# Optimization experiments

Hardware: AMD Instinct MI355X
Metric: run time of the kernel (lower is better)

## Reference

```python
import jax, jax.numpy as jnp
import numpy as np

N = 100_000   # nodes
C = 32        # classes
E = 3_200_000 # edges


def setup_inputs() -> dict:
    key = jax.random.key(0)
    k1, k2, k3, k4, k5 = jax.random.split(key, 5)
    edge_index = jax.random.randint(k1, (2, E), 0, N, dtype=jnp.int32)
    edge_weight = jax.random.uniform(k2, (E,), dtype=jnp.float32) + 0.1  # positive weights
    inputs = jax.random.normal(k3, (N, C), dtype=jnp.float32)
    labels = jax.random.randint(k4, (N,), 0, C)
    y = jax.nn.one_hot(labels, C, dtype=jnp.float32)  # torch.where(y[:, i]) implies one-hot labels
    sample_mask = jax.random.bernoulli(k5, 0.5, (N,))
    return {"edge_index": edge_index, "edge_weight": edge_weight,
            "inputs": inputs, "y": y, "sample_mask": sample_mask}


def _normalize_sparse(edge_index, edge_weight, n):
    # normalize_sparse_tensor: add self-loops (weight 1), then D^{-1/2} A D^{-1/2}
    loop = jnp.arange(n, dtype=edge_index.dtype)
    row = jnp.concatenate([edge_index[0], loop])
    col = jnp.concatenate([edge_index[1], loop])
    w = jnp.concatenate([edge_weight, jnp.ones((n,), edge_weight.dtype)])
    deg = jax.ops.segment_sum(w, row, num_segments=n)
    dinv = jnp.where(deg > 0, jax.lax.rsqrt(deg), 0.0)
    vals = dinv[row] * w * dinv[col]
    return row, col, vals


def reference(edge_index, edge_weight, inputs, y, sample_mask):
    n, c = inputs.shape
    row, col, vals = _normalize_sparse(edge_index, edge_weight, n)

    p = jax.nn.softmax(inputs, axis=1)
    m = sample_mask.astype(p.dtype)[:, None]
    p = p * (1.0 - m) + y * m          # replace predictions by labels on masked nodes
    ym = y * m                          # labels only on masked nodes

    # nodeH = raw_normed_adj @ p   (sparse spmm)  -> (n, c)
    nodeH = jax.ops.segment_sum(vals[:, None] * p[col], row, num_segments=n)

    # per-class mean of nodeH over nodes with label i (one-hot => sum/count)
    cnt = ym.sum(axis=0)                         # (c,)
    H = (ym.T @ nodeH) / cnt[:, None]            # (c, c); NaN rows if class empty

    # NaN fixups (identity when no NaNs present)
    Hn = jnp.isnan(H)
    H = jnp.where(Hn, H.T, H)
    Hn = jnp.isnan(H)
    H0 = jnp.where(Hn, jnp.zeros_like(H), H)
    miss = (1.0 - H0.sum(axis=1, keepdims=True)) / Hn.sum(axis=1, keepdims=True).astype(H.dtype)
    H = jnp.where(Hn, miss, H0)

    # makeDoubleStochasticH: iterate col-norm then row-norm; 'delta' = ||H||_1 (as in source)
    def cond(state):
        _, i, d = state
        return (d >= 1e-12) & (i < 3000)

    def body(state):
        Hc, i, _ = state
        Hc = Hc / Hc.sum(axis=0, keepdims=True)
        Hc = Hc / Hc.sum(axis=1, keepdims=True)
        return Hc, i + 1, jnp.abs(Hc).sum()

    H, _, _ = jax.lax.while_loop(cond, body, (H, jnp.int32(0), jnp.float32(1e30)))
    return H
```

## Files before the change

### kernel.cpp

```cpp
#include <hip/hip_runtime.h>
#include <hip/hip_fp16.h>


#define RS 40960
#define BDEG 80
#define W 200
#define NBKTMAX 512
#define BCAP 4608
#define LCAP 4096
#define NSC 512
#define NPR NBKTMAX
#define NTOT (1 + NPR)
#define NRED 16
#define RPER ((NTOT + NRED - 1) / NRED)
#define PPAD 204
#define BVW 3200

__global__ __launch_bounds__(1024) void
k_deg(const int* __restrict__ ei, const float* __restrict__ ew,
      __half* __restrict__ slab, const unsigned char* __restrict__ mask_bytes,
      int* __restrict__ flag, float* __restrict__ Hg, float* __restrict__ cnt,
      int* __restrict__ gCnt, int E_, int R, int Nn) {
  __shared__ float h[RS];
  if (blockIdx.x == 0) {
    Hg[threadIdx.x] = 0.f;
    if (threadIdx.x < 32) cnt[threadIdx.x] = 0.f;
    if (threadIdx.x < NBKTMAX) gCnt[threadIdx.x] = 0;
    int* hi = (int*)h;
    if (threadIdx.x == 0) hi[0] = 0;
    __syncthreads();
    int acc = mask_bytes[threadIdx.x * 4 + 1] | mask_bytes[threadIdx.x * 4 + 2]
            | mask_bytes[threadIdx.x * 4 + 3];
    if (acc) atomicOr(&hi[0], 1);
    __syncthreads();
    if (threadIdx.x == 0) *flag = (hi[0] != 0) ? 1 : 0;
  }
  int g = blockIdx.x >> 3, xx = blockIdx.x & 7;
  int r = g % R;
  int sl = xx + 8 * (g / R);
  int lo = r * RS;
  int used = min(RS, Nn - lo);
  for (int i = threadIdx.x; i < used; i += 1024) h[i] = 0.f;
  __syncthreads();
  int Q = E_ >> 2;
  int q0 = (int)((long long)Q * sl / BDEG);
  int q1 = (int)((long long)Q * (sl + 1) / BDEG);
  const int4* ei4 = (const int4*)ei;
  const float4* ew4 = (const float4*)ew;
  int q = q0 + threadIdx.x;
  for (; q + 1024 < q1; q += 2048) {
    int4 ia = ei4[q], ib = ei4[q + 1024];
    float4 wa = ew4[q], wb = ew4[q + 1024];
    unsigned o0 = (unsigned)(ia.x - lo), o1 = (unsigned)(ia.y - lo);
    unsigned o2 = (unsigned)(ia.z - lo), o3 = (unsigned)(ia.w - lo);
    unsigned o4 = (unsigned)(ib.x - lo), o5 = (unsigned)(ib.y - lo);
    unsigned o6 = (unsigned)(ib.z - lo), o7 = (unsigned)(ib.w - lo);
    if (o0 < RS) atomicAdd(&h[o0], wa.x);
    if (o1 < RS) atomicAdd(&h[o1], wa.y);
    if (o2 < RS) atomicAdd(&h[o2], wa.z);
    if (o3 < RS) atomicAdd(&h[o3], wa.w);
    if (o4 < RS) atomicAdd(&h[o4], wb.x);
    if (o5 < RS) atomicAdd(&h[o5], wb.y);
    if (o6 < RS) atomicAdd(&h[o6], wb.z);
    if (o7 < RS) atomicAdd(&h[o7], wb.w);
  }
  for (; q < q1; q += 1024) {
    int4 idx = ei4[q];
    float4 w = ew4[q];
    unsigned o0 = (unsigned)(idx.x - lo), o1 = (unsigned)(idx.y - lo);
    unsigned o2 = (unsigned)(idx.z - lo), o3 = (unsigned)(idx.w - lo);
    if (o0 < RS) atomicAdd(&h[o0], w.x);
    if (o1 < RS) atomicAdd(&h[o1], w.y);
    if (o2 < RS) atomicAdd(&h[o2], w.z);
    if (o3 < RS) atomicAdd(&h[o3], w.w);
  }
  if (sl == BDEG - 1) {
    for (int e = (Q << 2) + threadIdx.x; e < E_; e += 1024) {
      unsigned off = (unsigned)(ei[e] - lo);
      if (off < RS) atomicAdd(&h[off], ew[e]);
    }
  }
  __syncthreads();
  __half* dst = slab + ((size_t)r * BDEG + sl) * RS;
  for (int i = threadIdx.x; i < used; i += 1024) dst[i] = __float2half(h[i]);
}

__global__ void k_node(const float* __restrict__ x, const float* __restrict__ y,
                       const void* __restrict__ maskp, const int* __restrict__ flag,
                       const __half* __restrict__ slab, int2* __restrict__ ninfo,
                       __half* __restrict__ p16, float* __restrict__ Hg,
                       float* __restrict__ cnt, unsigned* __restrict__ bitvec, int Nn) {
  __shared__ float scnt[32], sdiag[32];
  if (threadIdx.x < 32) { scnt[threadIdx.x] = 0.f; sdiag[threadIdx.x] = 0.f; }
  __syncthreads();
  int n = blockIdx.x * blockDim.x + threadIdx.x;
  bool inb = (n < Nn);
  bool byteMask = (*flag != 0);
  bool msk = false;
  if (inb)
    msk = byteMask ? (((const unsigned char*)maskp)[n] != 0)
                   : (((const int*)maskp)[n] != 0);
  unsigned long long bm = __ballot(msk);
  if ((threadIdx.x & 63) == 0)
    ((unsigned long long*)bitvec)[n >> 6] = bm;
  if (inb) {
    const __half* sl = slab + ((size_t)(n / RS) * BDEG) * RS + (n % RS);
    float d = 0.f;
    #pragma unroll 5
    for (int bb = 0; bb < BDEG; ++bb) d += __half2float(sl[(size_t)bb * RS]);
    float dinv = rsqrtf(d + 1.0f);
    int a = -1;
    if (msk) {
      const float4* yi = (const float4*)(y + (size_t)n * 32);
      #pragma unroll
      for (int q = 0; q < 8; ++q) {
        float4 v = yi[q];
        if (v.x == 1.f) a = q * 4 + 0;
        if (v.y == 1.f) a = q * 4 + 1;
        if (v.z == 1.f) a = q * 4 + 2;
        if (v.w == 1.f) a = q * 4 + 3;
      }
      atomicAdd(&scnt[a], 1.f);
      atomicAdd(&sdiag[a], dinv * dinv);
    } else {
      const float4* xi = (const float4*)(x + (size_t)n * 32);
      float xs[32];
      #pragma unroll
      for (int q = 0; q < 8; ++q) {
        float4 v = xi[q];
        xs[q*4+0] = v.x; xs[q*4+1] = v.y; xs[q*4+2] = v.z; xs[q*4+3] = v.w;
      }
      float mx = -3.4e38f;
      #pragma unroll
      for (int i = 0; i < 32; ++i) mx = fmaxf(mx, xs[i]);
      float s = 0.f;
      #pragma unroll
      for (int i = 0; i < 32; ++i) { xs[i] = __expf(xs[i] - mx); s += xs[i]; }
      float inv = 1.f / s;
      union { short sh[32]; int4 v[4]; } u;
      #pragma unroll
      for (int i = 0; i < 32; ++i)
        u.sh[i] = __half_as_short(__float2half(xs[i] * inv));
      int4* po = (int4*)(p16 + (size_t)n * 32);
      #pragma unroll
      for (int q = 0; q < 4; ++q) po[q] = u.v[q];
    }
    int2 ni; ni.x = __float_as_int(dinv); ni.y = a;
    ninfo[n] = ni;
  }
  __syncthreads();
  if (threadIdx.x < 32) {
    if (scnt[threadIdx.x] != 0.f) atomicAdd(&cnt[threadIdx.x], scnt[threadIdx.x]);
    if (sdiag[threadIdx.x] != 0.f) atomicAdd(&Hg[threadIdx.x * 33], sdiag[threadIdx.x]);
  }
}

__global__ __launch_bounds__(1024) void
k_bucket(const int* __restrict__ ei, const float* __restrict__ ew,
         const int2* __restrict__ ninfo, const unsigned* __restrict__ bitvec,
         int2* __restrict__ gBucket, int* __restrict__ gCnt, int E_) {
  __shared__ int2 list[LCAP];
  __shared__ int lcnt;
  __shared__ int bcnt[NBKTMAX];
  __shared__ int gbase[NBKTMAX];
  __shared__ int bplace[NBKTMAX];
  __shared__ unsigned sbv[BVW];
  if (threadIdx.x == 0) lcnt = 0;
  if (threadIdx.x < NBKTMAX) { bcnt[threadIdx.x] = 0; bplace[threadIdx.x] = 0; }
  for (int i = threadIdx.x; i < BVW; i += 1024) sbv[i] = bitvec[i];
  __syncthreads();
  int E4 = E_ >> 2;
  int q0 = (int)((long long)E4 * blockIdx.x / NSC);
  int q1 = (int)((long long)E4 * (blockIdx.x + 1) / NSC);
  for (int q = q0 + threadIdx.x; q < q1; q += 1024) {
    int4 rr = ((const int4*)ei)[q];
    int4 cc = ((const int4*)(ei + E_))[q];
    float4 ww = ((const float4*)ew)[q];
    int rs[4] = {rr.x, rr.y, rr.z, rr.w};
    int cs[4] = {cc.x, cc.y, cc.z, cc.w};
    float wv[4] = {ww.x, ww.y, ww.z, ww.w};
    bool act[4];
    #pragma unroll
    for (int k = 0; k < 4; ++k)
      act[k] = (sbv[(unsigned)rs[k] >> 5] >> (rs[k] & 31)) & 1;
    int2 nr[4];
    #pragma unroll
    for (int k = 0; k < 4; ++k)
      if (act[k]) nr[k] = ninfo[rs[k]];
    #pragma unroll
    for (int k = 0; k < 4; ++k) {
      if (act[k]) {
        float val = __int_as_float(nr[k].x) * wv[k];
        int pos = atomicAdd(&lcnt, 1);
        if (pos < LCAP) list[pos] = make_int2((cs[k] << 5) | nr[k].y, __float_as_int(val));
      }
    }
  }
  if (blockIdx.x == NSC - 1) {
    for (int e = (E4 << 2) + threadIdx.x; e < E_; e += 1024) {
      int r = ei[e];
      if (!((sbv[(unsigned)r >> 5] >> (r & 31)) & 1)) continue;
      int2 nr = ninfo[r];
      int c = ei[E_ + e];
      float val = __int_as_float(nr.x) * ew[e];
      int pos = atomicAdd(&lcnt, 1);
      if (pos < LCAP) list[pos] = make_int2((c << 5) | nr.y, __float_as_int(val));
    }
  }
  __syncthreads();
  int nl = min(lcnt, LCAP);
  for (int i = threadIdx.x; i < nl; i += 1024)
    atomicAdd(&bcnt[(list[i].x >> 5) / W], 1);
  __syncthreads();
  if (threadIdx.x < NBKTMAX) {
    int n = bcnt[threadIdx.x];
    gbase[threadIdx.x] = (n > 0) ? atomicAdd(&gCnt[threadIdx.x], n) : 0;
  }
  __syncthreads();
  for (int i = threadIdx.x; i < nl; i += 1024) {
    int2 rec = list[i];
    int bkt = (rec.x >> 5) / W;
    int slot = atomicAdd(&bplace[bkt], 1);
    int dst = gbase[bkt] + slot;
    if (dst < BCAP) gBucket[(size_t)bkt * BCAP + dst] = rec;
  }
}

__global__ __launch_bounds__(1024) void
k_process(const int2* __restrict__ gBucket, const int* __restrict__ gCnt,
          const int2* __restrict__ ninfo, const __half* __restrict__ p16,
          float* __restrict__ procSlab, int Nn) {
  __shared__ float TlocT[32 * W];
  __shared__ __half plocT[32 * PPAD];
  __shared__ float H32[1024];
  __shared__ float ldin[W];
  __shared__ int   llab[W];
  __shared__ short cmap[W];
  __shared__ short cidx[W];
  __shared__ int   nUs;
  int k = blockIdx.x;
  int c0 = k * W;
  int Wb = min(c0 + W, Nn) - c0;
  H32[threadIdx.x] = 0.f;
  if ((int)threadIdx.x < Wb) {
    int2 ni = ninfo[c0 + threadIdx.x];
    ldin[threadIdx.x] = __int_as_float(ni.x);
    llab[threadIdx.x] = ni.y;
  }
  if (threadIdx.x == 0) nUs = 0;
  __syncthreads();
  if (threadIdx.x < 64) {
    int base = 0;
    for (int ch = 0; ch < W; ch += 64) {
      int j = ch + threadIdx.x;
      bool u = (j < Wb) && (llab[j] < 0);
      unsigned long long m = __ballot(u);
      int p = base + __popcll(m & ((1ull << threadIdx.x) - 1ull));
      if (u) { cmap[j] = (short)p; cidx[p] = (short)j; }
      base += (int)__popcll(m);
    }
    if (threadIdx.x == 0) nUs = base;
  }
  for (int i = threadIdx.x; i < 32 * W; i += 1024) TlocT[i] = 0.f;
  __syncthreads();
  int nU = nUs;
  if (Wb > 0) {
    for (int i = threadIdx.x; i < nU * 32; i += 1024) {
      int j = i >> 5, b = i & 31;
      plocT[b * PPAD + j] = p16[(size_t)(c0 + cidx[j]) * 32 + b];
    }
    int n = min(gCnt[k], BCAP);
    const int2* bk = gBucket + (size_t)k * BCAP;
    for (int i = threadIdx.x; i < n; i += 1024) {
      int2 rec = bk[i];
      int cl = (rec.x >> 5) - c0;
      int a = rec.x & 31;
      float v = __int_as_float(rec.y) * ldin[cl];
      int b = llab[cl];
      if (b >= 0) atomicAdd(&H32[a * 32 + b], v);
      else        atomicAdd(&TlocT[a * W + cmap[cl]], v);
    }
  }
  __syncthreads();
  int a = threadIdx.x >> 5;
  int b = threadIdx.x & 31;
  float acc0 = 0.f, acc1 = 0.f, acc2 = 0.f, acc3 = 0.f;
  int c = 0;
  for (; c + 3 < nU; c += 4) {
    float4 tv = *(const float4*)&TlocT[a * W + c];
    short4 ps = *(const short4*)&plocT[b * PPAD + c];
    acc0 += tv.x * __half2float(__short_as_half(ps.x));
    acc1 += tv.y * __half2float(__short_as_half(ps.y));
    acc2 += tv.z * __half2float(__short_as_half(ps.z));
    acc3 += tv.w * __half2float(__short_as_half(ps.w));
  }
  for (; c < nU; ++c)
    acc0 += TlocT[a * W + c] * __half2float(plocT[b * PPAD + c]);
  procSlab[(size_t)k * 1024 + threadIdx.x] =
      (acc0 + acc1) + (acc2 + acc3) + H32[threadIdx.x];
}

__global__ __launch_bounds__(1024) void
k_red(const float* __restrict__ allSlabs, float* __restrict__ red) {
  int k0 = blockIdx.x * RPER;
  int k1 = min(k0 + RPER, NTOT);
  float s = 0.f;
  for (int k = k0; k < k1; ++k) s += allSlabs[(size_t)k * 1024 + threadIdx.x];
  red[(size_t)blockIdx.x * 1024 + threadIdx.x] = s;
}

__global__ __launch_bounds__(1024) void
k_sinkhorn(const float* __restrict__ red, const float* __restrict__ cnt,
           float* __restrict__ out) {
  __shared__ float sHH[1024];
  int t = threadIdx.x;
  float s = 0.f;
  #pragma unroll
  for (int k = 0; k < NRED; ++k) s += red[(size_t)k * 1024 + t];
  sHH[t] = s;
  __syncthreads();
  int j = t;
  if (j >= 32) return;
  float cj = cnt[j];
  float Hcol[32], Hrow[32];
  #pragma unroll
  for (int i = 0; i < 32; ++i) Hcol[i] = sHH[i * 32 + j];
  #pragma unroll
  for (int i = 0; i < 32; ++i) Hcol[i] /= __shfl(cj, i);
  #pragma unroll
  for (int k = 0; k < 32; ++k) Hrow[k] = sHH[j * 32 + k] / cj;
  float u = 1.f, v = 1.f;
  for (int it = 0; it < 40; ++it) {
    float a0 = 0.f, a1 = 0.f, a2 = 0.f, a3 = 0.f;
    #pragma unroll
    for (int i = 0; i < 32; i += 4) {
      a0 += Hcol[i+0] * __shfl(u, i+0);
      a1 += Hcol[i+1] * __shfl(u, i+1);
      a2 += Hcol[i+2] * __shfl(u, i+2);
      a3 += Hcol[i+3] * __shfl(u, i+3);
    }
    v = 1.f / ((a0 + a1) + (a2 + a3));
    a0 = a1 = a2 = a3 = 0.f;
    #pragma unroll
    for (int k = 0; k < 32; k += 4) {
      a0 += Hrow[k+0] * __shfl(v, k+0);
      a1 += Hrow[k+1] * __shfl(v, k+1);
      a2 += Hrow[k+2] * __shfl(v, k+2);
      a3 += Hrow[k+3] * __shfl(v, k+3);
    }
    u = 1.f / ((a0 + a1) + (a2 + a3));
  }
  #pragma unroll
  for (int i = 0; i < 32; ++i) out[i * 32 + j] = __shfl(u, i) * Hcol[i] * v;
}

extern "C" void kernel_launch(void* const* d_in, const int* in_sizes, int n_in,
                              void* d_out, int out_size, void* d_ws, size_t ws_size,
                              hipStream_t stream) {
  const int*   ei   = (const int*)d_in[0];
  const float* ew   = (const float*)d_in[1];
  const float* x    = (const float*)d_in[2];
  const float* y    = (const float*)d_in[3];
  const void*  mask = d_in[4];
  float* out = (float*)d_out;
  int E_ = in_sizes[1];
  int Nn = in_sizes[2] / 32;
  int R = (Nn + RS - 1) / RS;

  char* ws = (char*)d_ws;
  size_t o = 0;
  float* cnt = (float*)(ws + o);    o += 128;
  int*   flag = (int*)(ws + o);     o += 128;
  int*   gCnt = (int*)(ws + o);     o += NBKTMAX * 4;
  float* allSlabs = (float*)(ws + o);
  float* Hg       = allSlabs;
  float* procSlab = allSlabs + 1024;
  o += (size_t)NTOT * 4096;
  float* red = (float*)(ws + o);    o += (size_t)NRED * 4096;
  int2*  gBucket = (int2*)(ws + o); o += (size_t)NBKTMAX * BCAP * 8;
  __half* slab = (__half*)(ws + o); o += (size_t)R * BDEG * RS * 2;
  int2*  ninfo = (int2*)(ws + o);   o += (size_t)Nn * 8;
  __half* p16 = (__half*)(ws + o);  o += (size_t)Nn * 64;
  unsigned* gbv = (unsigned*)(ws + o); o += (size_t)BVW * 4;

  int nb = (Nn + 255) / 256;
  k_deg<<<R * BDEG, 1024, 0, stream>>>(ei, ew, slab, (const unsigned char*)mask,
                                       flag, Hg, cnt, gCnt, E_, R, Nn);
  k_node<<<nb, 256, 0, stream>>>(x, y, mask, flag, slab, ninfo, p16, Hg, cnt, gbv, Nn);
  k_bucket<<<NSC, 1024, 0, stream>>>(ei, ew, ninfo, gbv, gBucket, gCnt, E_);
  k_process<<<NPR, 1024, 0, stream>>>(gBucket, gCnt, ninfo, p16, procSlab, Nn);
  k_red<<<NRED, 1024, 0, stream>>>(allSlabs, red);
  k_sinkhorn<<<1, 1024, 0, stream>>>(red, cnt, out);
}
```

Measured before the change: 216.6 us.

## Partition edges by row range before degree histogram to avoid redundant scans

```diff
diff --git a/kernel.cpp b/kernel.cpp
--- a/kernel.cpp
+++ b/kernel.cpp
@@ -15,73 +15,105 @@
 #define RPER ((NTOT + NRED - 1) / NRED)
 #define PPAD 204
 #define BVW 3200
-
-__global__ __launch_bounds__(1024) void
-k_deg(const int* __restrict__ ei, const float* __restrict__ ew,
-      __half* __restrict__ slab, const unsigned char* __restrict__ mask_bytes,
-      int* __restrict__ flag, float* __restrict__ Hg, float* __restrict__ cnt,
-      int* __restrict__ gCnt, int E_, int R, int Nn) {
-  __shared__ float h[RS];
+#define PCAP 1600000
+
+__global__ __launch_bounds__(1024) void
+k_part(const int* __restrict__ ei, const float* __restrict__ ew,
+       int2* __restrict__ part, int* __restrict__ partCnt,
+       const unsigned char* __restrict__ mask_bytes, int* __restrict__ flag,
+       float* __restrict__ Hg, float* __restrict__ cnt, int* __restrict__ gCnt, int E_) {
+  __shared__ int bcnt3[3], gbase3[3], bplace3[3];
+  __shared__ int shi;
   if (blockIdx.x == 0) {
     Hg[threadIdx.x] = 0.f;
     if (threadIdx.x < 32) cnt[threadIdx.x] = 0.f;
     if (threadIdx.x < NBKTMAX) gCnt[threadIdx.x] = 0;
-    int* hi = (int*)h;
-    if (threadIdx.x == 0) hi[0] = 0;
+    if (threadIdx.x == 0) shi = 0;
     __syncthreads();
     int acc = mask_bytes[threadIdx.x * 4 + 1] | mask_bytes[threadIdx.x * 4 + 2]
             | mask_bytes[threadIdx.x * 4 + 3];
-    if (acc) atomicOr(&hi[0], 1);
+    if (acc) atomicOr(&shi, 1);
     __syncthreads();
-    if (threadIdx.x == 0) *flag = (hi[0] != 0) ? 1 : 0;
-  }
-  int g = blockIdx.x >> 3, xx = blockIdx.x & 7;
-  int r = g % R;
-  int sl = xx + 8 * (g / R);
+    if (threadIdx.x == 0) *flag = (shi != 0) ? 1 : 0;
+  }
+  if (threadIdx.x < 3) { bcnt3[threadIdx.x] = 0; bplace3[threadIdx.x] = 0; }
+  __syncthreads();
+  int Q = E_ >> 2;
+  int q0 = (int)((long long)Q * blockIdx.x / NSC);
+  int q1 = (int)((long long)Q * (blockIdx.x + 1) / NSC);
+  const int4* ei4 = (const int4*)ei;
+  const float4* ew4 = (const float4*)ew;
+  int c0 = 0, c1 = 0, c2 = 0;
+  for (int q = q0 + threadIdx.x; q < q1; q += 1024) {
+    int4 n = ei4[q];
+    c0 += (n.x < RS) + (n.y < RS) + (n.z < RS) + (n.w < RS);
+    c2 += (n.x >= 2*RS) + (n.y >= 2*RS) + (n.z >= 2*RS) + (n.w >= 2*RS);
+    c1 += 4;
+  }
+  if (blockIdx.x == NSC - 1) {
+    for (int e = (Q << 2) + threadIdx.x; e < E_; e += 1024) {
+      int n = ei[e];
+      c0 += (n < RS); c2 += (n >= 2*RS); c1 += 1;
+    }
+  }
+  c1 -= c0 + c2;
+  #pragma unroll
+  for (int off = 32; off >= 1; off >>= 1) {
+    c0 += __shfl_down(c0, off);
+    c1 += __shfl_down(c1, off);
+    c2 += __shfl_down(c2, off);
+  }
+  if ((threadIdx.x & 63) == 0) {
+    atomicAdd(&bcnt3[0], c0); atomicAdd(&bcnt3[1], c1); atomicAdd(&bcnt3[2], c2);
+  }
+  __syncthreads();
+  if (threadIdx.x < 3)
+    gbase3[threadIdx.x] = atomicAdd(&partCnt[threadIdx.x], bcnt3[threadIdx.x]);
+  __syncthreads();
+  for (int q = q0 + threadIdx.x; q < q1; q += 1024) {
+    int4 n = ei4[q];
+    float4 w = ew4[q];
+    int ns[4] = {n.x, n.y, n.z, n.w};
+    float wv[4] = {w.x, w.y, w.z, w.w};
+    #pragma unroll
+    for (int k = 0; k < 4; ++k) {
+      int rng = (ns[k] >= 2*RS) ? 2 : ((ns[k] >= RS) ? 1 : 0);
+      int slot = gbase3[rng] + atomicAdd(&bplace3[rng], 1);
+      if (slot < PCAP)
+        part[(size_t)rng * PCAP + slot] = make_int2(ns[k], __float_as_int(wv[k]));
+    }
+  }
+  if (blockIdx.x == NSC - 1) {
+    for (int e = (Q << 2) + threadIdx.x; e < E_; e += 1024) {
+      int n = ei[e];
+      int rng = (n >= 2*RS) ? 2 : ((n >= RS) ? 1 : 0);
+      int slot = gbase3[rng] + atomicAdd(&bplace3[rng], 1);
+      if (slot < PCAP)
+        part[(size_t)rng * PCAP + slot] = make_int2(n, __float_as_int(ew[e]));
+    }
+  }
+}
+
+__global__ __launch_bounds__(1024) void
+k_deghist(const int2* __restrict__ part, const int* __restrict__ partCnt,
+          __half* __restrict__ slab, int Nn) {
+  __shared__ float h[RS];
+  int r = blockIdx.x / BDEG;
+  int s = blockIdx.x % BDEG;
   int lo = r * RS;
   int used = min(RS, Nn - lo);
   for (int i = threadIdx.x; i < used; i += 1024) h[i] = 0.f;
   __syncthreads();
-  int Q = E_ >> 2;
-  int q0 = (int)((long long)Q * sl / BDEG);
-  int q1 = (int)((long long)Q * (sl + 1) / BDEG);
-  const int4* ei4 = (const int4*)ei;
-  const float4* ew4 = (const float4*)ew;
-  int q = q0 + threadIdx.x;
-  for (; q + 1024 < q1; q += 2048) {
-    int4 ia = ei4[q], ib = ei4[q + 1024];
-    float4 wa = ew4[q], wb = ew4[q + 1024];
-    unsigned o0 = (unsigned)(ia.x - lo), o1 = (unsigned)(ia.y - lo);
-    unsigned o2 = (unsigned)(ia.z - lo), o3 = (unsigned)(ia.w - lo);
-    unsigned o4 = (unsigned)(ib.x - lo), o5 = (unsigned)(ib.y - lo);
-    unsigned o6 = (unsigned)(ib.z - lo), o7 = (unsigned)(ib.w - lo);
-    if (o0 < RS) atomicAdd(&h[o0], wa.x);
-    if (o1 < RS) atomicAdd(&h[o1], wa.y);
-    if (o2 < RS) atomicAdd(&h[o2], wa.z);
-    if (o3 < RS) atomicAdd(&h[o3], wa.w);
-    if (o4 < RS) atomicAdd(&h[o4], wb.x);
-    if (o5 < RS) atomicAdd(&h[o5], wb.y);
-    if (o6 < RS) atomicAdd(&h[o6], wb.z);
-    if (o7 < RS) atomicAdd(&h[o7], wb.w);
-  }
-  for (; q < q1; q += 1024) {
-    int4 idx = ei4[q];
-    float4 w = ew4[q];
-    unsigned o0 = (unsigned)(idx.x - lo), o1 = (unsigned)(idx.y - lo);
-    unsigned o2 = (unsigned)(idx.z - lo), o3 = (unsigned)(idx.w - lo);
-    if (o0 < RS) atomicAdd(&h[o0], w.x);
-    if (o1 < RS) atomicAdd(&h[o1], w.y);
-    if (o2 < RS) atomicAdd(&h[o2], w.z);
-    if (o3 < RS) atomicAdd(&h[o3], w.w);
-  }
-  if (sl == BDEG - 1) {
-    for (int e = (Q << 2) + threadIdx.x; e < E_; e += 1024) {
-      unsigned off = (unsigned)(ei[e] - lo);
-      if (off < RS) atomicAdd(&h[off], ew[e]);
-    }
-  }
-  __syncthreads();
-  __half* dst = slab + ((size_t)r * BDEG + sl) * RS;
+  int cr = min(partCnt[r], PCAP);
+  int i0 = (int)((long long)cr * s / BDEG);
+  int i1 = (int)((long long)cr * (s + 1) / BDEG);
+  const int2* pr = part + (size_t)r * PCAP;
+  for (int i = i0 + threadIdx.x; i < i1; i += 1024) {
+    int2 rec = pr[i];
+    atomicAdd(&h[rec.x - lo], __int_as_float(rec.y));
+  }
+  __syncthreads();
+  __half* dst = slab + ((size_t)r * BDEG + s) * RS;
   for (int i = threadIdx.x; i < used; i += 1024) dst[i] = __float2half(h[i]);
 }
 
@@ -371,6 +403,7 @@
   size_t o = 0;
   float* cnt = (float*)(ws + o);    o += 128;
   int*   flag = (int*)(ws + o);     o += 128;
+  int*   partCnt = (int*)(ws + o);  o += 128;
   int*   gCnt = (int*)(ws + o);     o += NBKTMAX * 4;
   float* allSlabs = (float*)(ws + o);
   float* Hg       = allSlabs;
@@ -382,10 +415,13 @@
   int2*  ninfo = (int2*)(ws + o);   o += (size_t)Nn * 8;
   __half* p16 = (__half*)(ws + o);  o += (size_t)Nn * 64;
   unsigned* gbv = (unsigned*)(ws + o); o += (size_t)BVW * 4;
+  int2*  part = (int2*)(ws + o);    o += (size_t)3 * PCAP * 8;
 
   int nb = (Nn + 255) / 256;
-  k_deg<<<R * BDEG, 1024, 0, stream>>>(ei, ew, slab, (const unsigned char*)mask,
-                                       flag, Hg, cnt, gCnt, E_, R, Nn);
+  hipMemsetAsync(partCnt, 0, 128, stream);
+  k_part<<<NSC, 1024, 0, stream>>>(ei, ew, part, partCnt, (const unsigned char*)mask,
+                                   flag, Hg, cnt, gCnt, E_);
+  k_deghist<<<R * BDEG, 1024, 0, stream>>>(part, partCnt, slab, Nn);
   k_node<<<nb, 256, 0, stream>>>(x, y, mask, flag, slab, ninfo, p16, Hg, cnt, gbv, Nn);
   k_bucket<<<NSC, 1024, 0, stream>>>(ei, ew, ninfo, gbv, gBucket, gCnt, E_);
   k_process<<<NPR, 1024, 0, stream>>>(gBucket, gCnt, ninfo, p16, procSlab, Nn);
```

Result: slower. 239.2 us (+10.4%).
